# Kernel optimization log

Measured on AMD Instinct MI355X. Metric: run time of the kernel, lower is better.

Reference implementation:

```python
import jax, jax.numpy as jnp
import numpy as np

DIM = 1024
NUM_HEADS = 16
HEAD_DIM = DIM // NUM_HEADS
B, S, E = 4, 8192, 2000


def setup_inputs() -> dict:
    key = jax.random.key(0)
    ks = jax.random.split(key, 16)
    sd = 0.02
    inp = {
        "x": jax.random.normal(ks[0], (B, S, DIM), dtype=jnp.float32),
        "src_indices": jax.random.randint(ks[1], (E,), 0, S),
        "dst_indices": jax.random.randint(ks[2], (E,), 0, S),
        # linear weights stored [in, out] (applied as x @ W + b)
        "Wq": jax.random.normal(ks[3], (DIM, DIM), jnp.float32) * sd,
        "bq": jnp.zeros((DIM,), jnp.float32),
        "Wk": jax.random.normal(ks[4], (DIM, DIM), jnp.float32) * sd,
        "bk": jnp.zeros((DIM,), jnp.float32),
        "Wv": jax.random.normal(ks[5], (DIM, DIM), jnp.float32) * sd,
        "bv": jnp.zeros((DIM,), jnp.float32),
        "Wo": jax.random.normal(ks[6], (DIM, DIM), jnp.float32) * sd,
        "bo": jnp.zeros((DIM,), jnp.float32),
        "edge_weight": jax.random.normal(ks[7], (1, NUM_HEADS, 1), jnp.float32),
        "W1": jax.random.normal(ks[8], (2 * HEAD_DIM, HEAD_DIM), jnp.float32) * sd,
        "b1": jnp.zeros((HEAD_DIM,), jnp.float32),
        "W2": jax.random.normal(ks[9], (HEAD_DIM, 1), jnp.float32) * sd,
        "b2": jnp.zeros((1,), jnp.float32),
    }
    return inp


def reference(x, src_indices, dst_indices, Wq, bq, Wk, bk, Wv, bv, Wo, bo,
              edge_weight, W1, b1, W2, b2):
    Bs, Sl, D = x.shape
    H, hd = NUM_HEADS, HEAD_DIM
    scale = hd ** -0.5

    def heads(t):  # [B,S,D] -> [B,H,S,hd]
        return t.reshape(Bs, Sl, H, hd).transpose(0, 2, 1, 3)

    q = heads(x @ Wq + bq)
    k = heads(x @ Wk + bk)
    v = heads(x @ Wv + bv)

    q_src = jnp.take(q, src_indices, axis=2)   # [B,H,E,hd]
    k_dst = jnp.take(k, dst_indices, axis=2)   # [B,H,E,hd]
    v_dst = jnp.take(v, dst_indices, axis=2)   # [B,H,E,hd]

    ef = jnp.concatenate([q_src, k_dst], axis=-1)          # [B,H,E,2hd]
    h = jax.nn.gelu(ef @ W1 + b1, approximate=False)       # [B,H,E,hd]
    scores = (h @ W2 + b2) * scale                         # [B,H,E,1]
    attn = jax.nn.softmax(scores, axis=2)                  # softmax over all edges
    attn = attn * edge_weight[..., None]                   # [1,H,1,1] broadcast

    weighted = attn * v_dst                                # [B,H,E,hd]
    out = jnp.zeros((Bs, H, Sl, hd), x.dtype).at[:, :, src_indices, :].add(weighted)

    final = out.transpose(0, 2, 1, 3).reshape(Bs, Sl, D)
    return final @ Wo + bo
```

## Files before the change

### kernel.cpp

```cpp
#include <hip/hip_runtime.h>
#include <hip/hip_bf16.h>
#include <math.h>

#define DIMK 1024
#define NH 16
#define HD 64
#define BB 4
#define SS 8192
#define EPAD 136
#define NKT 32

typedef __attribute__((ext_vector_type(8))) short bf16x8;
typedef __attribute__((ext_vector_type(8))) unsigned short ushort8;
typedef __attribute__((ext_vector_type(4))) unsigned short us4;
typedef __attribute__((ext_vector_type(4))) float f32x4;

#define MFMA16(a, b, c) __builtin_amdgcn_mfma_f32_16x16x32_bf16((a), (b), (c), 0, 0, 0)

__device__ __forceinline__ unsigned short f32_to_bf16_rne(float f) {
  unsigned int u = __float_as_uint(f);
  u = (u + 0x7fffu + ((u >> 16) & 1u)) >> 16;
  return (unsigned short)u;
}
__device__ __forceinline__ float bf16_bits_to_f32(unsigned short b) {
  return __uint_as_float(((unsigned int)b) << 16);
}
__device__ __forceinline__ void gload16(const void* g, void* l) {
  __builtin_amdgcn_global_load_lds((const __attribute__((address_space(1))) void*)g,
                                   (__attribute__((address_space(3))) void*)l, 16, 0, 0);
}

__global__ __launch_bounds__(256) void fill_out_kernel(const float4* __restrict__ bo4,
                                                       float4* __restrict__ out, int total4) {
  for (int i = blockIdx.x * 256 + threadIdx.x; i < total4; i += gridDim.x * 256)
    out[i] = bo4[i & 255];
}

__global__ __launch_bounds__(256) void prep_w4(
    const float* __restrict__ Wq, const float* __restrict__ Wk,
    const float* __restrict__ Wv, const float* __restrict__ Wo,
    unsigned short* __restrict__ Bq, unsigned short* __restrict__ Bkv,
    unsigned short* __restrict__ Bo) {
  const float* W;
  unsigned short* Bpan;
  int pnoff;
  switch (blockIdx.z) {
    case 0: W = Wq; Bpan = Bq; pnoff = 0; break;
    case 1: W = Wk; Bpan = Bkv; pnoff = 0; break;
    case 2: W = Wv; Bpan = Bkv; pnoff = 8; break;
    default: W = Wo; Bpan = Bo; pnoff = 0; break;
  }
  __shared__ float st[64][65];
  const int bk = blockIdx.x * 64, bn = blockIdx.y * 64;
  const int t = threadIdx.x;
  const int lr = t >> 4, lc = (t & 15) * 4;
#pragma unroll
  for (int i = 0; i < 4; i++) {
    int k = lr + i * 16;
    float4 v = *(const float4*)(W + (size_t)(bk + k) * DIMK + bn + lc);
    st[k][lc] = v.x; st[k][lc + 1] = v.y; st[k][lc + 2] = v.z; st[k][lc + 3] = v.w;
  }
  __syncthreads();
  const int ktile = (bk + lc) >> 5, c = lc & 31;
#pragma unroll
  for (int i = 0; i < 4; i++) {
    const int nl = lr + i * 16;
    const int n = bn + nl;
    const int r = n & 127, pn = (n >> 7) + pnoff;
    const int q = (c >> 3) ^ ((r >> 1) & 3);
    const size_t byteoff = (size_t)r * 64 + q * 16 + (c & 7) * 2;
    us4 hv, lv;
#pragma unroll
    for (int j = 0; j < 4; j++) {
      float v = st[lc + j][nl];
      unsigned short hb = f32_to_bf16_rne(v);
      hv[j] = hb;
      lv[j] = f32_to_bf16_rne(v - bf16_bits_to_f32(hb));
    }
    char* base = (char*)Bpan;
    *(us4*)(base + (((size_t)pn * 64 + ktile) << 13) + byteoff) = hv;
    *(us4*)(base + (((size_t)pn * 64 + 32 + ktile) << 13) + byteoff) = lv;
  }
}

__global__ __launch_bounds__(256) void prep_w1(const float* __restrict__ W1,
                                               unsigned short* __restrict__ W1Th,
                                               unsigned short* __restrict__ W1Tl) {
  for (int idx = threadIdx.x; idx < 128 * 64; idx += 256) {
    int k = idx >> 6, n = idx & 63;
    float v = W1[idx];
    unsigned short hb = f32_to_bf16_rne(v);
    W1Th[n * 128 + k] = hb;
    W1Tl[n * 128 + k] = f32_to_bf16_rne(v - bf16_bits_to_f32(hb));
  }
}

__global__ __launch_bounds__(256) void prep_a(const float* __restrict__ X,
                                              const int* __restrict__ gidx,
                                              unsigned short* __restrict__ Apan, int M, int E) {
  const int row = blockIdx.x;
  const int r = row & 255, mt = row >> 8;
  const int c0 = threadIdx.x * 4;
  const int kt = c0 >> 5, c = c0 & 31;
  const int q = (c >> 3) ^ ((r >> 1) & 3);
  const size_t byteoff = (size_t)r * 64 + q * 16 + (c & 7) * 2;
  char* base = (char*)Apan;
  us4 hv = (us4){0, 0, 0, 0}, lv = (us4){0, 0, 0, 0};
  if (row < M) {
    const float* sr;
    if (gidx) {
      int b = row / E, e = row - b * E;
      sr = X + ((size_t)b * SS + gidx[e]) * DIMK;
    } else {
      sr = X + (size_t)row * DIMK;
    }
    float4 v = *(const float4*)(sr + c0);
    float vv[4] = {v.x, v.y, v.z, v.w};
#pragma unroll
    for (int i = 0; i < 4; i++) {
      unsigned short hb = f32_to_bf16_rne(vv[i]);
      hv[i] = hb;
      lv[i] = f32_to_bf16_rne(vv[i] - bf16_bits_to_f32(hb));
    }
  }
  *(us4*)(base + (((size_t)(mt * 64 + kt)) << 14) + byteoff) = hv;
  *(us4*)(base + (((size_t)(mt * 64 + 32 + kt)) << 14) + byteoff) = lv;
}

__global__ __launch_bounds__(1024) void first_occ(const int* __restrict__ src,
                                                  int* __restrict__ fidx,
                                                  int* __restrict__ mark, int E) {
  __shared__ int tbl[SS];
  for (int i = threadIdx.x; i < SS; i += 1024) tbl[i] = 0x7fffffff;
  __syncthreads();
  for (int e = threadIdx.x; e < E; e += 1024) atomicMin(&tbl[src[e]], e);
  __syncthreads();
  for (int e = threadIdx.x; e < E; e += 1024) mark[e] = 0;
  __syncthreads();
  for (int e = threadIdx.x; e < E; e += 1024) {
    int f = tbl[src[e]];
    fidx[e] = f;
    if (f != e) mark[f] = 1;
  }
}

template <int BN, int MODE>
__global__ __launch_bounds__(512, 2) void gemm8(
    const unsigned short* __restrict__ Apan, const unsigned short* __restrict__ Bpan,
    const float* __restrict__ bias, const float* __restrict__ bias2,
    float* __restrict__ out, int ldc, int nty,
    const int* __restrict__ fidx, const int* __restrict__ srci, int M, int E) {
  constexpr int NF = BN / 64;
  constexpr int BT = BN * 32;
  __shared__ unsigned short ldsAh[2][8192];
  __shared__ unsigned short ldsAl[2][8192];
  __shared__ unsigned short ldsBh[2][BT];
  __shared__ unsigned short ldsBl[2][BT];

  const int tid = threadIdx.x, lane = tid & 63, wv = tid >> 6;
  const int wr = wv >> 2, wc = wv & 3;

  const int w = (blockIdx.x & 7) * ((int)gridDim.x >> 3) + ((int)blockIdx.x >> 3);
  const int mt = w / nty, nt_ = w - mt * nty;
  const int m0 = mt * 256, n0 = nt_ * BN;

  const int rr = lane & 15, lq = lane >> 4;
  const int swz = (rr >> 1) & 3;
  const int aoff = (wr * 128 + rr) * 32 + ((lq ^ swz) << 3);
  const int boff = (wc * (BN / 4) + rr) * 32 + ((lq ^ swz) << 3);

  const char* Apb = (const char*)Apan + ((size_t)(mt * 64) << 14);
  const char* Bpb = (const char*)Bpan;
  const int stoff = wv * 1024 + lane * 16;

  f32x4 acc[8][NF];
#pragma unroll
  for (int i = 0; i < 8; i++)
#pragma unroll
    for (int j = 0; j < NF; j++) acc[i][j] = (f32x4){0.f, 0.f, 0.f, 0.f};

  auto stage = [&](int kt, int buf) {
    const char* sAh = Apb + ((size_t)kt << 14) + stoff;
    const char* sAl = Apb + ((size_t)(32 + kt) << 14) + stoff;
    gload16(sAh, &ldsAh[buf][wv * 512]);
    gload16(sAh + 8192, &ldsAh[buf][wv * 512 + 4096]);
    gload16(sAl, &ldsAl[buf][wv * 512]);
    gload16(sAl + 8192, &ldsAl[buf][wv * 512 + 4096]);
    if (BN == 256) {
      const char* sB0h = Bpb + (((size_t)(2 * nt_) * 64 + kt) << 13) + stoff;
      const char* sB1h = Bpb + (((size_t)(2 * nt_ + 1) * 64 + kt) << 13) + stoff;
      const char* sB0l = Bpb + (((size_t)(2 * nt_) * 64 + 32 + kt) << 13) + stoff;
      const char* sB1l = Bpb + (((size_t)(2 * nt_ + 1) * 64 + 32 + kt) << 13) + stoff;
      gload16(sB0h, &ldsBh[buf][wv * 512]);
      gload16(sB1h, &ldsBh[buf][wv * 512 + 4096]);
      gload16(sB0l, &ldsBl[buf][wv * 512]);
      gload16(sB1l, &ldsBl[buf][wv * 512 + 4096]);
    } else {
      const char* sBh = Bpb + (((size_t)nt_ * 64 + kt) << 13) + stoff;
      const char* sBl = Bpb + (((size_t)nt_ * 64 + 32 + kt) << 13) + stoff;
      gload16(sBh, &ldsBh[buf][wv * 512]);
      gload16(sBl, &ldsBl[buf][wv * 512]);
    }
  };

  stage(0, 0);
  asm volatile("s_waitcnt vmcnt(0)" ::: "memory");
  __builtin_amdgcn_sched_barrier(0);
  __builtin_amdgcn_s_barrier();

  for (int kt = 0; kt < NKT; ++kt) {
    const int buf = kt & 1;
    const unsigned short* Ah = ldsAh[buf];
    const unsigned short* Al = ldsAl[buf];
    const unsigned short* Bh = ldsBh[buf];
    const unsigned short* Bl = ldsBl[buf];

    bf16x8 fbh[NF], fah[8], fal[8], fbl[NF];
#pragma unroll
    for (int nf = 0; nf < NF; ++nf) fbh[nf] = *(const bf16x8*)(Bh + boff + nf * 512);
#pragma unroll
    for (int mf = 0; mf < 8; ++mf) fah[mf] = *(const bf16x8*)(Ah + aoff + mf * 512);
    __builtin_amdgcn_sched_barrier(0);
#pragma unroll
    for (int mf = 0; mf < 8; ++mf) fal[mf] = *(const bf16x8*)(Al + aoff + mf * 512);
    __builtin_amdgcn_sched_barrier(0);
#pragma unroll
    for (int nf = 0; nf < NF; ++nf) fbl[nf] = *(const bf16x8*)(Bl + boff + nf * 512);
    __builtin_amdgcn_sched_barrier(0);

    if (kt + 1 < NKT) stage(kt + 1, buf ^ 1);

    asm volatile("s_waitcnt lgkmcnt(%0)" ::"i"(8 + NF) : "memory");
    __builtin_amdgcn_sched_barrier(0);
    __builtin_amdgcn_s_setprio(1);
#pragma unroll
    for (int mf = 0; mf < 8; ++mf)
#pragma unroll
      for (int nf = 0; nf < NF; ++nf) acc[mf][nf] = MFMA16(fah[mf], fbh[nf], acc[mf][nf]);
    __builtin_amdgcn_s_setprio(0);

    asm volatile("s_waitcnt lgkmcnt(%0)" ::"i"(NF) : "memory");
    __builtin_amdgcn_sched_barrier(0);
    __builtin_amdgcn_s_setprio(1);
#pragma unroll
    for (int mf = 0; mf < 8; ++mf)
#pragma unroll
      for (int nf = 0; nf < NF; ++nf) acc[mf][nf] = MFMA16(fal[mf], fbh[nf], acc[mf][nf]);
    __builtin_amdgcn_s_setprio(0);

    asm volatile("s_waitcnt lgkmcnt(0)" ::: "memory");
    if (kt + 1 < NKT) {
      asm volatile("s_waitcnt vmcnt(0)" ::: "memory");
      __builtin_amdgcn_sched_barrier(0);
      __builtin_amdgcn_s_barrier();
    } else {
      __builtin_amdgcn_sched_barrier(0);
    }

    __builtin_amdgcn_s_setprio(1);
#pragma unroll
    for (int mf = 0; mf < 8; ++mf)
#pragma unroll
      for (int nf = 0; nf < NF; ++nf) acc[mf][nf] = MFMA16(fah[mf], fbl[nf], acc[mf][nf]);
    __builtin_amdgcn_s_setprio(0);
  }

  const int cq = lane >> 4, cr = lane & 15;
#pragma unroll
  for (int nf = 0; nf < NF; ++nf) {
    const int col = n0 + wc * (BN / 4) + nf * 16 + cr;
    const float bv = (MODE == 0 && bias2 != nullptr && col >= DIMK) ? bias2[col - DIMK]
                                                                    : bias[col & (DIMK - 1)];
#pragma unroll
    for (int mf = 0; mf < 8; ++mf) {
#pragma unroll
      for (int r = 0; r < 4; ++r) {
        const int mrow = m0 + wr * 128 + mf * 16 + cq * 4 + r;
        if (mrow >= M) continue;
        if (MODE == 0) {
          out[(size_t)mrow * ldc + col] = acc[mf][nf][r] + bv;
        } else {
          int b = mrow / E, e = mrow - b * E;
          if (fidx[e] == e) {
            int orow = b * SS + srci[e];
            out[(size_t)orow * ldc + col] = acc[mf][nf][r] + bv;
          }
        }
      }
    }
  }
}

__global__ __launch_bounds__(256) void edge_scores_mfma(
    const float* __restrict__ qs, const float* __restrict__ kd, int ldk,
    const unsigned short* __restrict__ W1Th, const unsigned short* __restrict__ W1Tl,
    const float* __restrict__ b1, const float* __restrict__ W2,
    const float* __restrict__ b2, float* __restrict__ scores, int E, int CH) {
  __shared__ unsigned short W1h[64][EPAD], W1l[64][EPAD];
  __shared__ unsigned short EFh[4][16][EPAD], EFl[4][16][EPAD];
  const int tid = threadIdx.x, lane = tid & 63, w = tid >> 6;
  const int bh = blockIdx.x / CH, ch = blockIdx.x - bh * CH;
  const int b = bh >> 4, h = bh & 15;

  for (int idx = tid; idx < 64 * 16; idx += 256) {
    int n = idx >> 4, g = (idx & 15) * 8;
    *(ushort8*)&W1h[n][g] = *(const ushort8*)(W1Th + n * 128 + g);
    *(ushort8*)&W1l[n][g] = *(const ushort8*)(W1Tl + n * 128 + g);
  }
  __syncthreads();

  const int etile = ch * 4 + w;
  const int e0 = etile * 16;
  if (e0 >= E) return;

  const int r = lane >> 2, c0 = (lane & 3) * 16;
  {
    const int er = (e0 + r < E) ? e0 + r : E - 1;
    const float* qrow = qs + ((size_t)(b * E + er)) * DIMK + h * HD + c0;
    const float* krow = kd + ((size_t)(b * E + er)) * (size_t)ldk + h * HD + c0;
    float qv[16], kvv[16];
#pragma unroll
    for (int i = 0; i < 4; i++) {
      *(float4*)&qv[i * 4] = *(const float4*)(qrow + i * 4);
      *(float4*)&kvv[i * 4] = *(const float4*)(krow + i * 4);
    }
    ushort8 qh[2], ql[2], kh[2], kl[2];
#pragma unroll
    for (int g = 0; g < 2; g++)
#pragma unroll
      for (int i = 0; i < 8; i++) {
        float v = qv[g * 8 + i];
        unsigned short hb = f32_to_bf16_rne(v);
        qh[g][i] = hb;
        ql[g][i] = f32_to_bf16_rne(v - bf16_bits_to_f32(hb));
        float v2 = kvv[g * 8 + i];
        unsigned short hb2 = f32_to_bf16_rne(v2);
        kh[g][i] = hb2;
        kl[g][i] = f32_to_bf16_rne(v2 - bf16_bits_to_f32(hb2));
      }
    *(ushort8*)&EFh[w][r][c0] = qh[0];
    *(ushort8*)&EFh[w][r][c0 + 8] = qh[1];
    *(ushort8*)&EFl[w][r][c0] = ql[0];
    *(ushort8*)&EFl[w][r][c0 + 8] = ql[1];
    *(ushort8*)&EFh[w][r][64 + c0] = kh[0];
    *(ushort8*)&EFh[w][r][64 + c0 + 8] = kh[1];
    *(ushort8*)&EFl[w][r][64 + c0] = kl[0];
    *(ushort8*)&EFl[w][r][64 + c0 + 8] = kl[1];
  }
  asm volatile("s_waitcnt lgkmcnt(0)" ::: "memory");
  __builtin_amdgcn_sched_barrier(0);

  f32x4 acc[4];
#pragma unroll
  for (int i = 0; i < 4; i++) acc[i] = (f32x4){0.f, 0.f, 0.f, 0.f};

  const int kk = (lane >> 4) * 8, rrl = lane & 15;
#pragma unroll
  for (int ks = 0; ks < 4; ks++) {
    bf16x8 ah = *(bf16x8*)&EFh[w][rrl][ks * 32 + kk];
    bf16x8 al = *(bf16x8*)&EFl[w][rrl][ks * 32 + kk];
#pragma unroll
    for (int nf = 0; nf < 4; nf++) {
      bf16x8 bh_ = *(bf16x8*)&W1h[nf * 16 + rrl][ks * 32 + kk];
      bf16x8 bl_ = *(bf16x8*)&W1l[nf * 16 + rrl][ks * 32 + kk];
      acc[nf] = MFMA16(ah, bh_, acc[nf]);
      acc[nf] = MFMA16(ah, bl_, acc[nf]);
      acc[nf] = MFMA16(al, bh_, acc[nf]);
    }
  }

  const int col_l = lane & 15, rq = lane >> 4;
  float w2v[4], b1v[4];
#pragma unroll
  for (int nf = 0; nf < 4; nf++) {
    w2v[nf] = W2[nf * 16 + col_l];
    b1v[nf] = b1[nf * 16 + col_l];
  }
  float p[4];
#pragma unroll
  for (int rr2 = 0; rr2 < 4; rr2++) {
    float s = 0.f;
#pragma unroll
    for (int nf = 0; nf < 4; nf++) {
      float hv = acc[nf][rr2] + b1v[nf];
      hv = 0.5f * hv * (1.f + erff(hv * 0.70710678118654752f));
      s = fmaf(hv, w2v[nf], s);
    }
    p[rr2] = s;
  }
#pragma unroll
  for (int off = 1; off < 16; off <<= 1)
#pragma unroll
    for (int rr2 = 0; rr2 < 4; rr2++) p[rr2] += __shfl_xor(p[rr2], off, 64);

  if (col_l == 0) {
    const float b2v = b2[0];
#pragma unroll
    for (int rr2 = 0; rr2 < 4; rr2++) {
      int e = e0 + rq * 4 + rr2;
      if (e < E) scores[(size_t)(b * NH + h) * E + e] = (p[rr2] + b2v) * 0.125f;
    }
  }
}

__global__ __launch_bounds__(256) void softmax_ew(float* __restrict__ scores,
                                                  const float* __restrict__ ew, int E) {
  const int row = blockIdx.x;
  const int h = row & (NH - 1);
  float* s = scores + (size_t)row * E;
  const int tid = threadIdx.x, lane = tid & 63, w = tid >> 6;
  __shared__ float red[4];

  float vals[8];
  float mx = -1e30f;
#pragma unroll
  for (int i = 0; i < 8; i++) {
    int j = tid + i * 256;
    vals[i] = (j < E) ? s[j] : -1e30f;
    mx = fmaxf(mx, vals[i]);
  }
#pragma unroll
  for (int off = 32; off; off >>= 1) mx = fmaxf(mx, __shfl_xor(mx, off, 64));
  if (lane == 0) red[w] = mx;
  __syncthreads();
  mx = fmaxf(fmaxf(red[0], red[1]), fmaxf(red[2], red[3]));
  __syncthreads();

  float sum = 0.f;
#pragma unroll
  for (int i = 0; i < 8; i++) {
    vals[i] = __expf(vals[i] - mx);
    if (tid + i * 256 < E) sum += vals[i];
  }
#pragma unroll
  for (int off = 32; off; off >>= 1) sum += __shfl_xor(sum, off, 64);
  if (lane == 0) red[w] = sum;
  __syncthreads();
  sum = red[0] + red[1] + red[2] + red[3];

  const float scaleout = ew[h] / sum;
#pragma unroll
  for (int i = 0; i < 8; i++) {
    int j = tid + i * 256;
    if (j < E) s[j] = vals[i] * scaleout;
  }
}

__global__ __launch_bounds__(256) void weight_split(
    const float* __restrict__ vd, int ldv, const float* __restrict__ attn,
    float* __restrict__ wrow, unsigned short* __restrict__ Apan, int M, int E) {
  const int row = blockIdx.x;
  const int r = row & 255, mt = row >> 8;
  const int c0 = threadIdx.x * 4;
  const int kt = c0 >> 5, c = c0 & 31;
  const int q = (c >> 3) ^ ((r >> 1) & 3);
  const size_t byteoff = (size_t)r * 64 + q * 16 + (c & 7) * 2;
  char* base = (char*)Apan;
  us4 hv = (us4){0, 0, 0, 0}, lv = (us4){0, 0, 0, 0};
  if (row < M) {
    const int b = row / E, e = row - b * E;
    const float a = attn[(size_t)(b * NH + (c0 >> 6)) * E + e];
    float4 v = *(const float4*)(vd + (size_t)row * ldv + c0);
    v.x *= a; v.y *= a; v.z *= a; v.w *= a;
    *(float4*)(wrow + (size_t)row * DIMK + c0) = v;
    float vv[4] = {v.x, v.y, v.z, v.w};
#pragma unroll
    for (int i = 0; i < 4; i++) {
      unsigned short hb = f32_to_bf16_rne(vv[i]);
      hv[i] = hb;
      lv[i] = f32_to_bf16_rne(vv[i] - bf16_bits_to_f32(hb));
    }
  }
  *(us4*)(base + (((size_t)(mt * 64 + kt)) << 14) + byteoff) = hv;
  *(us4*)(base + (((size_t)(mt * 64 + 32 + kt)) << 14) + byteoff) = lv;
}

__global__ __launch_bounds__(256) void dup_add(const int* __restrict__ f,
                                               float* __restrict__ wrow, int E) {
  const int e = blockIdx.x;
  const int fe = f[e];
  if (fe == e) return;
  const int d = threadIdx.x * 4;
#pragma unroll
  for (int b = 0; b < BB; b++) {
    const float4 v = *(const float4*)(wrow + (size_t)(b * E + e) * DIMK + d);
    float* dst = wrow + (size_t)(b * E + fe) * DIMK + d;
    atomicAdd(dst + 0, v.x);
    atomicAdd(dst + 1, v.y);
    atomicAdd(dst + 2, v.z);
    atomicAdd(dst + 3, v.w);
  }
}

__global__ __launch_bounds__(256) void dup_fix(const int* __restrict__ fidx,
                                               const int* __restrict__ mark,
                                               const float* __restrict__ wrow,
                                               unsigned short* __restrict__ Apan, int E) {
  const int e = blockIdx.x;
  if (fidx[e] != e || !mark[e]) return;
  const int c0 = threadIdx.x * 4;
  const int kt = c0 >> 5, c = c0 & 31;
  char* base = (char*)Apan;
  for (int b = 0; b < BB; b++) {
    const int row = b * E + e;
    const int r = row & 255, mt = row >> 8;
    const int q = (c >> 3) ^ ((r >> 1) & 3);
    const size_t byteoff = (size_t)r * 64 + q * 16 + (c & 7) * 2;
    float4 v = *(const float4*)(wrow + (size_t)row * DIMK + c0);
    float vv[4] = {v.x, v.y, v.z, v.w};
    us4 hv, lv;
#pragma unroll
    for (int i = 0; i < 4; i++) {
      unsigned short hb = f32_to_bf16_rne(vv[i]);
      hv[i] = hb;
      lv[i] = f32_to_bf16_rne(vv[i] - bf16_bits_to_f32(hb));
    }
    *(us4*)(base + (((size_t)(mt * 64 + kt)) << 14) + byteoff) = hv;
    *(us4*)(base + (((size_t)(mt * 64 + 32 + kt)) << 14) + byteoff) = lv;
  }
}

extern "C" void kernel_launch(void* const* d_in, const int* in_sizes, int n_in,
                              void* d_out, int out_size, void* d_ws, size_t ws_size,
                              hipStream_t stream) {
  const float* x = (const float*)d_in[0];
  const int* src = (const int*)d_in[1];
  const int* dst = (const int*)d_in[2];
  const float* Wq = (const float*)d_in[3];
  const float* bq = (const float*)d_in[4];
  const float* Wk = (const float*)d_in[5];
  const float* bk = (const float*)d_in[6];
  const float* Wv = (const float*)d_in[7];
  const float* bv = (const float*)d_in[8];
  const float* Wo = (const float*)d_in[9];
  const float* bo = (const float*)d_in[10];
  const float* ew = (const float*)d_in[11];
  const float* W1 = (const float*)d_in[12];
  const float* b1 = (const float*)d_in[13];
  const float* W2 = (const float*)d_in[14];
  const float* b2 = (const float*)d_in[15];
  float* out = (float*)d_out;

  const int E = in_sizes[1];
  const int M = BB * E;
  const int gx = (M + 255) / 256;
  const int Mpad = gx * 256;

  char* w = (char*)d_ws;
  float* qs = (float*)w; w += (size_t)M * DIMK * 4;
  float* kv = (float*)w; w += (size_t)M * 2048 * 4;
  float* sc = (float*)w; w += (size_t)BB * NH * E * 4;
  int* fidx = (int*)w; w += (((size_t)E * 4) + 255) & ~(size_t)255;
  int* mark = (int*)w; w += (((size_t)E * 4) + 255) & ~(size_t)255;
  unsigned short* W1Th = (unsigned short*)w; w += 64 * 128 * 2;
  unsigned short* W1Tl = (unsigned short*)w; w += 64 * 128 * 2;
  unsigned short* Bq = (unsigned short*)w; w += (size_t)8 * 64 * 8192;
  unsigned short* Bkv = (unsigned short*)w; w += (size_t)16 * 64 * 8192;
  unsigned short* Bo = (unsigned short*)w; w += (size_t)8 * 64 * 8192;
  unsigned short* Apan = (unsigned short*)w; w += (size_t)gx * 64 * 16384;

  float* wrow = qs;

  const int total4 = BB * SS * (DIMK / 4);
  fill_out_kernel<<<2048, 256, 0, stream>>>((const float4*)bo, (float4*)out, total4);

  prep_w4<<<dim3(16, 16, 4), 256, 0, stream>>>(Wq, Wk, Wv, Wo, Bq, Bkv, Bo);
  prep_w1<<<1, 256, 0, stream>>>(W1, W1Th, W1Tl);

  first_occ<<<1, 1024, 0, stream>>>(src, fidx, mark, E);

  prep_a<<<Mpad, 256, 0, stream>>>(x, src, Apan, M, E);
  gemm8<128, 0><<<gx * 8, 512, 0, stream>>>(Apan, Bq, bq, nullptr, qs, DIMK, 8,
                                            nullptr, nullptr, M, E);

  prep_a<<<Mpad, 256, 0, stream>>>(x, dst, Apan, M, E);
  gemm8<256, 0><<<gx * 8, 512, 0, stream>>>(Apan, Bkv, bk, bv, kv, 2048, 8,
                                            nullptr, nullptr, M, E);

  const int etiles = (E + 15) / 16;
  const int CH = (etiles + 3) / 4;
  edge_scores_mfma<<<BB * NH * CH, 256, 0, stream>>>(qs, kv, 2048, W1Th, W1Tl, b1, W2, b2,
                                                     sc, E, CH);
  softmax_ew<<<BB * NH, 256, 0, stream>>>(sc, ew, E);

  weight_split<<<Mpad, 256, 0, stream>>>(kv + 1024, 2048, sc, wrow, Apan, M, E);
  dup_add<<<E, 256, 0, stream>>>(fidx, wrow, E);
  dup_fix<<<E, 256, 0, stream>>>(fidx, mark, wrow, Apan, E);

  gemm8<128, 1><<<gx * 8, 512, 0, stream>>>(Apan, Bo, bo, nullptr, out, DIMK, 8,
                                            fidx, src, M, E);
}
```

Baseline: 344.9 us.

## Fold W1 into Q/K projection weights and simplify edge score kernel

```diff
diff --git a/kernel.cpp b/kernel.cpp
--- a/kernel.cpp
+++ b/kernel.cpp
@@ -7,7 +7,6 @@
 #define HD 64
 #define BB 4
 #define SS 8192
-#define EPAD 136
 #define NKT 32
 
 typedef __attribute__((ext_vector_type(8))) short bf16x8;
@@ -36,20 +35,12 @@
     out[i] = bo4[i & 255];
 }
 
-__global__ __launch_bounds__(256) void prep_w4(
-    const float* __restrict__ Wq, const float* __restrict__ Wk,
+__global__ __launch_bounds__(256) void prep_w2(
     const float* __restrict__ Wv, const float* __restrict__ Wo,
-    unsigned short* __restrict__ Bq, unsigned short* __restrict__ Bkv,
-    unsigned short* __restrict__ Bo) {
-  const float* W;
-  unsigned short* Bpan;
-  int pnoff;
-  switch (blockIdx.z) {
-    case 0: W = Wq; Bpan = Bq; pnoff = 0; break;
-    case 1: W = Wk; Bpan = Bkv; pnoff = 0; break;
-    case 2: W = Wv; Bpan = Bkv; pnoff = 8; break;
-    default: W = Wo; Bpan = Bo; pnoff = 0; break;
-  }
+    unsigned short* __restrict__ Bkv, unsigned short* __restrict__ Bo) {
+  const float* W = blockIdx.z ? Wo : Wv;
+  unsigned short* Bpan = blockIdx.z ? Bo : Bkv;
+  const int pnoff = blockIdx.z ? 0 : 8;
   __shared__ float st[64][65];
   const int bk = blockIdx.x * 64, bn = blockIdx.y * 64;
   const int t = threadIdx.x;
@@ -83,16 +74,70 @@
   }
 }
 
-__global__ __launch_bounds__(256) void prep_w1(const float* __restrict__ W1,
-                                               unsigned short* __restrict__ W1Th,
-                                               unsigned short* __restrict__ W1Tl) {
-  for (int idx = threadIdx.x; idx < 128 * 64; idx += 256) {
-    int k = idx >> 6, n = idx & 63;
-    float v = W1[idx];
-    unsigned short hb = f32_to_bf16_rne(v);
-    W1Th[n * 128 + k] = hb;
-    W1Tl[n * 128 + k] = f32_to_bf16_rne(v - bf16_bits_to_f32(hb));
-  }
+__global__ __launch_bounds__(256) void prep_wfold(
+    const float* __restrict__ Wq, const float* __restrict__ Wk,
+    const float* __restrict__ W1,
+    unsigned short* __restrict__ Bq, unsigned short* __restrict__ Bkv) {
+  const int which = blockIdx.z;
+  const float* W = which ? Wk : Wq;
+  unsigned short* Bpan = which ? Bkv : Bq;
+  const int d_off = which ? 64 : 0;
+  const int cc = blockIdx.x, jc = blockIdx.y;
+  __shared__ float Wb[64][65];
+  __shared__ float W1b[64][65];
+  const int t = threadIdx.x;
+  for (int idx = t; idx < 64 * 64; idx += 256) {
+    int rrow = idx >> 6, dd = idx & 63;
+    Wb[rrow][dd] = W[(size_t)(cc * 64 + rrow) * DIMK + jc * 64 + dd];
+    W1b[rrow][dd] = W1[(size_t)(d_off + rrow) * 64 + dd];
+  }
+  __syncthreads();
+  const int n = t & 63, g0 = t >> 6;
+  const int pn = jc >> 1;
+  const int r = (jc & 1) * 64 + n;
+  const int sw = (r >> 1) & 3;
+  char* base = (char*)Bpan;
+#pragma unroll
+  for (int i = 0; i < 4; ++i) {
+    const int cl0 = (g0 + 4 * i) * 4;
+    float a0 = 0.f, a1 = 0.f, a2 = 0.f, a3 = 0.f;
+    for (int d = 0; d < 64; ++d) {
+      const float w1v = W1b[d][n];
+      a0 = fmaf(Wb[cl0 + 0][d], w1v, a0);
+      a1 = fmaf(Wb[cl0 + 1][d], w1v, a1);
+      a2 = fmaf(Wb[cl0 + 2][d], w1v, a2);
+      a3 = fmaf(Wb[cl0 + 3][d], w1v, a3);
+    }
+    float av[4] = {a0, a1, a2, a3};
+    const int c = cc * 64 + cl0;
+    const int kt = c >> 5, kcol = c & 31;
+    const int q = (kcol >> 3) ^ sw;
+    const size_t byteoff = (size_t)r * 64 + q * 16 + (kcol & 7) * 2;
+    us4 hv, lv;
+#pragma unroll
+    for (int j = 0; j < 4; j++) {
+      unsigned short hb = f32_to_bf16_rne(av[j]);
+      hv[j] = hb;
+      lv[j] = f32_to_bf16_rne(av[j] - bf16_bits_to_f32(hb));
+    }
+    *(us4*)(base + (((size_t)pn * 64 + kt) << 13) + byteoff) = hv;
+    *(us4*)(base + (((size_t)pn * 64 + 32 + kt) << 13) + byteoff) = lv;
+  }
+}
+
+__global__ __launch_bounds__(256) void prep_bias(
+    const float* __restrict__ bq, const float* __restrict__ bk,
+    const float* __restrict__ b1, const float* __restrict__ W1,
+    float* __restrict__ bqf, float* __restrict__ bkf) {
+  const int j = blockIdx.x * 256 + threadIdx.x;
+  const int h = j >> 6, n = j & 63;
+  float sq = 0.f, sk = 0.f;
+  for (int d = 0; d < 64; ++d) {
+    sq = fmaf(bq[h * 64 + d], W1[d * 64 + n], sq);
+    sk = fmaf(bk[h * 64 + d], W1[(64 + d) * 64 + n], sk);
+  }
+  bqf[j] = sq;
+  bkf[j] = sk + b1[n];
 }
 
 __global__ __launch_bounds__(256) void prep_a(const float* __restrict__ X,
@@ -144,38 +189,41 @@
   }
 }
 
-template <int BN, int MODE>
-__global__ __launch_bounds__(512, 2) void gemm8(
+template <int BM, int MODE>
+__global__ __launch_bounds__(512, 2) void gemmT(
     const unsigned short* __restrict__ Apan, const unsigned short* __restrict__ Bpan,
     const float* __restrict__ bias, const float* __restrict__ bias2,
     float* __restrict__ out, int ldc, int nty,
     const int* __restrict__ fidx, const int* __restrict__ srci, int M, int E) {
-  constexpr int NF = BN / 64;
-  constexpr int BT = BN * 32;
-  __shared__ unsigned short ldsAh[2][8192];
-  __shared__ unsigned short ldsAl[2][8192];
-  __shared__ unsigned short ldsBh[2][BT];
-  __shared__ unsigned short ldsBl[2][BT];
+  constexpr int MF = BM / 32;
+  constexpr int NF = 4;
+  constexpr int AT = BM * 32;
+  __shared__ unsigned short ldsAh[2][AT];
+  __shared__ unsigned short ldsAl[2][AT];
+  __shared__ unsigned short ldsBh[2][8192];
+  __shared__ unsigned short ldsBl[2][8192];
 
   const int tid = threadIdx.x, lane = tid & 63, wv = tid >> 6;
   const int wr = wv >> 2, wc = wv & 3;
 
   const int w = (blockIdx.x & 7) * ((int)gridDim.x >> 3) + ((int)blockIdx.x >> 3);
-  const int mt = w / nty, nt_ = w - mt * nty;
-  const int m0 = mt * 256, n0 = nt_ * BN;
+  const int mi = w / nty, nt_ = w - mi * nty;
+  const int m0 = mi * BM, n0 = nt_ * 256;
 
   const int rr = lane & 15, lq = lane >> 4;
   const int swz = (rr >> 1) & 3;
-  const int aoff = (wr * 128 + rr) * 32 + ((lq ^ swz) << 3);
-  const int boff = (wc * (BN / 4) + rr) * 32 + ((lq ^ swz) << 3);
-
-  const char* Apb = (const char*)Apan + ((size_t)(mt * 64) << 14);
+  const int aoff = (wr * (BM / 2) + rr) * 32 + ((lq ^ swz) << 3);
+  const int boff = (wc * 64 + rr) * 32 + ((lq ^ swz) << 3);
+
+  const int pt = (BM == 256) ? mi : (mi >> 1);
+  const int rowbase = (BM == 256) ? 0 : (mi & 1) * 128;
+  const char* Apb = (const char*)Apan + (((size_t)pt * 64) << 14) + (size_t)rowbase * 64;
   const char* Bpb = (const char*)Bpan;
   const int stoff = wv * 1024 + lane * 16;
 
-  f32x4 acc[8][NF];
-#pragma unroll
-  for (int i = 0; i < 8; i++)
+  f32x4 acc[MF][NF];
+#pragma unroll
+  for (int i = 0; i < MF; i++)
 #pragma unroll
     for (int j = 0; j < NF; j++) acc[i][j] = (f32x4){0.f, 0.f, 0.f, 0.f};
 
@@ -183,24 +231,19 @@
     const char* sAh = Apb + ((size_t)kt << 14) + stoff;
     const char* sAl = Apb + ((size_t)(32 + kt) << 14) + stoff;
     gload16(sAh, &ldsAh[buf][wv * 512]);
-    gload16(sAh + 8192, &ldsAh[buf][wv * 512 + 4096]);
     gload16(sAl, &ldsAl[buf][wv * 512]);
-    gload16(sAl + 8192, &ldsAl[buf][wv * 512 + 4096]);
-    if (BN == 256) {
-      const char* sB0h = Bpb + (((size_t)(2 * nt_) * 64 + kt) << 13) + stoff;
-      const char* sB1h = Bpb + (((size_t)(2 * nt_ + 1) * 64 + kt) << 13) + stoff;
-      const char* sB0l = Bpb + (((size_t)(2 * nt_) * 64 + 32 + kt) << 13) + stoff;
-      const char* sB1l = Bpb + (((size_t)(2 * nt_ + 1) * 64 + 32 + kt) << 13) + stoff;
-      gload16(sB0h, &ldsBh[buf][wv * 512]);
-      gload16(sB1h, &ldsBh[buf][wv * 512 + 4096]);
-      gload16(sB0l, &ldsBl[buf][wv * 512]);
-      gload16(sB1l, &ldsBl[buf][wv * 512 + 4096]);
-    } else {
-      const char* sBh = Bpb + (((size_t)nt_ * 64 + kt) << 13) + stoff;
-      const char* sBl = Bpb + (((size_t)nt_ * 64 + 32 + kt) << 13) + stoff;
-      gload16(sBh, &ldsBh[buf][wv * 512]);
-      gload16(sBl, &ldsBl[buf][wv * 512]);
-    }
+    if (BM == 256) {
+      gload16(sAh + 8192, &ldsAh[buf][wv * 512 + 4096]);
+      gload16(sAl + 8192, &ldsAl[buf][wv * 512 + 4096]);
+    }
+    const char* sB0h = Bpb + (((size_t)(2 * nt_) * 64 + kt) << 13) + stoff;
+    const char* sB1h = Bpb + (((size_t)(2 * nt_ + 1) * 64 + kt) << 13) + stoff;
+    const char* sB0l = Bpb + (((size_t)(2 * nt_) * 64 + 32 + kt) << 13) + stoff;
+    const char* sB1l = Bpb + (((size_t)(2 * nt_ + 1) * 64 + 32 + kt) << 13) + stoff;
+    gload16(sB0h, &ldsBh[buf][wv * 512]);
+    gload16(sB1h, &ldsBh[buf][wv * 512 + 4096]);
+    gload16(sB0l, &ldsBl[buf][wv * 512]);
+    gload16(sB1l, &ldsBl[buf][wv * 512 + 4096]);
   };
 
   stage(0, 0);
@@ -215,14 +258,14 @@
     const unsigned short* Bh = ldsBh[buf];
     const unsigned short* Bl = ldsBl[buf];
 
-    bf16x8 fbh[NF], fah[8], fal[8], fbl[NF];
+    bf16x8 fbh[NF], fah[MF], fal[MF], fbl[NF];
 #pragma unroll
     for (int nf = 0; nf < NF; ++nf) fbh[nf] = *(const bf16x8*)(Bh + boff + nf * 512);
 #pragma unroll
-    for (int mf = 0; mf < 8; ++mf) fah[mf] = *(const bf16x8*)(Ah + aoff + mf * 512);
+    for (int mf = 0; mf < MF; ++mf) fah[mf] = *(const bf16x8*)(Ah + aoff + mf * 512);
     __builtin_amdgcn_sched_barrier(0);
 #pragma unroll
-    for (int mf = 0; mf < 8; ++mf) fal[mf] = *(const bf16x8*)(Al + aoff + mf * 512);
+    for (int mf = 0; mf < MF; ++mf) fal[mf] = *(const bf16x8*)(Al + aoff + mf * 512);
     __builtin_amdgcn_sched_barrier(0);
 #pragma unroll
     for (int nf = 0; nf < NF; ++nf) fbl[nf] = *(const bf16x8*)(Bl + boff + nf * 512);
@@ -230,11 +273,11 @@
 
     if (kt + 1 < NKT) stage(kt + 1, buf ^ 1);
 
-    asm volatile("s_waitcnt lgkmcnt(%0)" ::"i"(8 + NF) : "memory");
+    asm volatile("s_waitcnt lgkmcnt(%0)" ::"i"(MF + NF) : "memory");
     __builtin_amdgcn_sched_barrier(0);
     __builtin_amdgcn_s_setprio(1);
 #pragma unroll
-    for (int mf = 0; mf < 8; ++mf)
+    for (int mf = 0; mf < MF; ++mf)
 #pragma unroll
       for (int nf = 0; nf < NF; ++nf) acc[mf][nf] = MFMA16(fah[mf], fbh[nf], acc[mf][nf]);
     __builtin_amdgcn_s_setprio(0);
@@ -243,7 +286,7 @@
     __builtin_amdgcn_sched_barrier(0);
     __builtin_amdgcn_s_setprio(1);
 #pragma unroll
-    for (int mf = 0; mf < 8; ++mf)
+    for (int mf = 0; mf < MF; ++mf)
 #pragma unroll
       for (int nf = 0; nf < NF; ++nf) acc[mf][nf] = MFMA16(fal[mf], fbh[nf], acc[mf][nf]);
     __builtin_amdgcn_s_setprio(0);
@@ -259,7 +302,7 @@
 
     __builtin_amdgcn_s_setprio(1);
 #pragma unroll
-    for (int mf = 0; mf < 8; ++mf)
+    for (int mf = 0; mf < MF; ++mf)
 #pragma unroll
       for (int nf = 0; nf < NF; ++nf) acc[mf][nf] = MFMA16(fah[mf], fbl[nf], acc[mf][nf]);
     __builtin_amdgcn_s_setprio(0);
@@ -268,14 +311,14 @@
   const int cq = lane >> 4, cr = lane & 15;
 #pragma unroll
   for (int nf = 0; nf < NF; ++nf) {
-    const int col = n0 + wc * (BN / 4) + nf * 16 + cr;
+    const int col = n0 + wc * 64 + nf * 16 + cr;
     const float bv = (MODE == 0 && bias2 != nullptr && col >= DIMK) ? bias2[col - DIMK]
                                                                     : bias[col & (DIMK - 1)];
 #pragma unroll
-    for (int mf = 0; mf < 8; ++mf) {
+    for (int mf = 0; mf < MF; ++mf) {
 #pragma unroll
       for (int r = 0; r < 4; ++r) {
-        const int mrow = m0 + wr * 128 + mf * 16 + cq * 4 + r;
+        const int mrow = m0 + wr * (BM / 2) + mf * 16 + cq * 4 + r;
         if (mrow >= M) continue;
         if (MODE == 0) {
           out[(size_t)mrow * ldc + col] = acc[mf][nf][r] + bv;
@@ -291,115 +334,26 @@
   }
 }
 
-__global__ __launch_bounds__(256) void edge_scores_mfma(
-    const float* __restrict__ qs, const float* __restrict__ kd, int ldk,
-    const unsigned short* __restrict__ W1Th, const unsigned short* __restrict__ W1Tl,
-    const float* __restrict__ b1, const float* __restrict__ W2,
-    const float* __restrict__ b2, float* __restrict__ scores, int E, int CH) {
-  __shared__ unsigned short W1h[64][EPAD], W1l[64][EPAD];
-  __shared__ unsigned short EFh[4][16][EPAD], EFl[4][16][EPAD];
+__global__ __launch_bounds__(256) void edge_scores_f(
+    const float* __restrict__ hq, const float* __restrict__ hk,
+    const float* __restrict__ W2, const float* __restrict__ b2,
+    float* __restrict__ scores, int E, int CH) {
   const int tid = threadIdx.x, lane = tid & 63, w = tid >> 6;
   const int bh = blockIdx.x / CH, ch = blockIdx.x - bh * CH;
   const int b = bh >> 4, h = bh & 15;
-
-  for (int idx = tid; idx < 64 * 16; idx += 256) {
-    int n = idx >> 4, g = (idx & 15) * 8;
-    *(ushort8*)&W1h[n][g] = *(const ushort8*)(W1Th + n * 128 + g);
-    *(ushort8*)&W1l[n][g] = *(const ushort8*)(W1Tl + n * 128 + g);
-  }
-  __syncthreads();
-
-  const int etile = ch * 4 + w;
-  const int e0 = etile * 16;
-  if (e0 >= E) return;
-
-  const int r = lane >> 2, c0 = (lane & 3) * 16;
-  {
-    const int er = (e0 + r < E) ? e0 + r : E - 1;
-    const float* qrow = qs + ((size_t)(b * E + er)) * DIMK + h * HD + c0;
-    const float* krow = kd + ((size_t)(b * E + er)) * (size_t)ldk + h * HD + c0;
-    float qv[16], kvv[16];
-#pragma unroll
-    for (int i = 0; i < 4; i++) {
-      *(float4*)&qv[i * 4] = *(const float4*)(qrow + i * 4);
-      *(float4*)&kvv[i * 4] = *(const float4*)(krow + i * 4);
-    }
-    ushort8 qh[2], ql[2], kh[2], kl[2];
-#pragma unroll
-    for (int g = 0; g < 2; g++)
-#pragma unroll
-      for (int i = 0; i < 8; i++) {
-        float v = qv[g * 8 + i];
-        unsigned short hb = f32_to_bf16_rne(v);
-        qh[g][i] = hb;
-        ql[g][i] = f32_to_bf16_rne(v - bf16_bits_to_f32(hb));
-        float v2 = kvv[g * 8 + i];
-        unsigned short hb2 = f32_to_bf16_rne(v2);
-        kh[g][i] = hb2;
-        kl[g][i] = f32_to_bf16_rne(v2 - bf16_bits_to_f32(hb2));
-      }
-    *(ushort8*)&EFh[w][r][c0] = qh[0];
-    *(ushort8*)&EFh[w][r][c0 + 8] = qh[1];
-    *(ushort8*)&EFl[w][r][c0] = ql[0];
-    *(ushort8*)&EFl[w][r][c0 + 8] = ql[1];
-    *(ushort8*)&EFh[w][r][64 + c0] = kh[0];
-    *(ushort8*)&EFh[w][r][64 + c0 + 8] = kh[1];
-    *(ushort8*)&EFl[w][r][64 + c0] = kl[0];
-    *(ushort8*)&EFl[w][r][64 + c0 + 8] = kl[1];
-  }
-  asm volatile("s_waitcnt lgkmcnt(0)" ::: "memory");
-  __builtin_amdgcn_sched_barrier(0);
-
-  f32x4 acc[4];
-#pragma unroll
-  for (int i = 0; i < 4; i++) acc[i] = (f32x4){0.f, 0.f, 0.f, 0.f};
-
-  const int kk = (lane >> 4) * 8, rrl = lane & 15;
-#pragma unroll
-  for (int ks = 0; ks < 4; ks++) {
-    bf16x8 ah = *(bf16x8*)&EFh[w][rrl][ks * 32 + kk];
-    bf16x8 al = *(bf16x8*)&EFl[w][rrl][ks * 32 + kk];
-#pragma unroll
-    for (int nf = 0; nf < 4; nf++) {
-      bf16x8 bh_ = *(bf16x8*)&W1h[nf * 16 + rrl][ks * 32 + kk];
-      bf16x8 bl_ = *(bf16x8*)&W1l[nf * 16 + rrl][ks * 32 + kk];
-      acc[nf] = MFMA16(ah, bh_, acc[nf]);
-      acc[nf] = MFMA16(ah, bl_, acc[nf]);
-      acc[nf] = MFMA16(al, bh_, acc[nf]);
-    }
-  }
-
-  const int col_l = lane & 15, rq = lane >> 4;
-  float w2v[4], b1v[4];
-#pragma unroll
-  for (int nf = 0; nf < 4; nf++) {
-    w2v[nf] = W2[nf * 16 + col_l];
-    b1v[nf] = b1[nf * 16 + col_l];
-  }
-  float p[4];
-#pragma unroll
-  for (int rr2 = 0; rr2 < 4; rr2++) {
-    float s = 0.f;
-#pragma unroll
-    for (int nf = 0; nf < 4; nf++) {
-      float hv = acc[nf][rr2] + b1v[nf];
-      hv = 0.5f * hv * (1.f + erff(hv * 0.70710678118654752f));
-      s = fmaf(hv, w2v[nf], s);
-    }
-    p[rr2] = s;
-  }
-#pragma unroll
-  for (int off = 1; off < 16; off <<= 1)
-#pragma unroll
-    for (int rr2 = 0; rr2 < 4; rr2++) p[rr2] += __shfl_xor(p[rr2], off, 64);
-
-  if (col_l == 0) {
-    const float b2v = b2[0];
-#pragma unroll
-    for (int rr2 = 0; rr2 < 4; rr2++) {
-      int e = e0 + rq * 4 + rr2;
-      if (e < E) scores[(size_t)(b * NH + h) * E + e] = (p[rr2] + b2v) * 0.125f;
-    }
+  const float w2 = W2[lane];
+  const float b2v = b2[0];
+#pragma unroll
+  for (int i = 0; i < 8; ++i) {
+    const int e = ch * 32 + w * 8 + i;
+    if (e >= E) break;
+    const size_t row = (size_t)(b * E + e);
+    float hv = hq[row * 1024 + h * 64 + lane] + hk[row * 2048 + h * 64 + lane];
+    hv = 0.5f * hv * (1.f + erff(hv * 0.70710678118654752f));
+    float p = hv * w2;
+#pragma unroll
+    for (int off = 32; off; off >>= 1) p += __shfl_xor(p, off, 64);
+    if (lane == 0) scores[(size_t)(b * NH + h) * E + e] = (p + b2v) * 0.125f;
   }
 }
 
@@ -545,6 +499,7 @@
   const int M = BB * E;
   const int gx = (M + 255) / 256;
   const int Mpad = gx * 256;
+  const int mi128 = gx * 2;
 
   char* w = (char*)d_ws;
   float* qs = (float*)w; w += (size_t)M * DIMK * 4;
@@ -552,8 +507,8 @@
   float* sc = (float*)w; w += (size_t)BB * NH * E * 4;
   int* fidx = (int*)w; w += (((size_t)E * 4) + 255) & ~(size_t)255;
   int* mark = (int*)w; w += (((size_t)E * 4) + 255) & ~(size_t)255;
-  unsigned short* W1Th = (unsigned short*)w; w += 64 * 128 * 2;
-  unsigned short* W1Tl = (unsigned short*)w; w += 64 * 128 * 2;
+  float* bqf = (float*)w; w += 1024 * 4;
+  float* bkf = (float*)w; w += 1024 * 4;
   unsigned short* Bq = (unsigned short*)w; w += (size_t)8 * 64 * 8192;
   unsigned short* Bkv = (unsigned short*)w; w += (size_t)16 * 64 * 8192;
   unsigned short* Bo = (unsigned short*)w; w += (size_t)8 * 64 * 8192;
@@ -564,29 +519,28 @@
   const int total4 = BB * SS * (DIMK / 4);
   fill_out_kernel<<<2048, 256, 0, stream>>>((const float4*)bo, (float4*)out, total4);
 
-  prep_w4<<<dim3(16, 16, 4), 256, 0, stream>>>(Wq, Wk, Wv, Wo, Bq, Bkv, Bo);
-  prep_w1<<<1, 256, 0, stream>>>(W1, W1Th, W1Tl);
+  prep_w2<<<dim3(16, 16, 2), 256, 0, stream>>>(Wv, Wo, Bkv, Bo);
+  prep_wfold<<<dim3(16, 16, 2), 256, 0, stream>>>(Wq, Wk, W1, Bq, Bkv);
+  prep_bias<<<4, 256, 0, stream>>>(bq, bk, b1, W1, bqf, bkf);
 
   first_occ<<<1, 1024, 0, stream>>>(src, fidx, mark, E);
 
   prep_a<<<Mpad, 256, 0, stream>>>(x, src, Apan, M, E);
-  gemm8<128, 0><<<gx * 8, 512, 0, stream>>>(Apan, Bq, bq, nullptr, qs, DIMK, 8,
+  gemmT<128, 0><<<mi128 * 4, 512, 0, stream>>>(Apan, Bq, bqf, nullptr, qs, DIMK, 4,
+                                               nullptr, nullptr, M, E);
+
+  prep_a<<<Mpad, 256, 0, stream>>>(x, dst, Apan, M, E);
+  gemmT<256, 0><<<gx * 8, 512, 0, stream>>>(Apan, Bkv, bkf, bv, kv, 2048, 8,
                                             nullptr, nullptr, M, E);
 
-  prep_a<<<Mpad, 256, 0, stream>>>(x, dst, Apan, M, E);
-  gemm8<256, 0><<<gx * 8, 512, 0, stream>>>(Apan, Bkv, bk, bv, kv, 2048, 8,
-                                            nullptr, nullptr, M, E);
-
-  const int etiles = (E + 15) / 16;
-  const int CH = (etiles + 3) / 4;
-  edge_scores_mfma<<<BB * NH * CH, 256, 0, stream>>>(qs, kv, 2048, W1Th, W1Tl, b1, W2, b2,
-                                                     sc, E, CH);
+  const int CH = (E + 31) / 32;
+  edge_scores_f<<<BB * NH * CH, 256, 0, stream>>>(qs, kv, W2, b2, sc, E, CH);
   softmax_ew<<<BB * NH, 256, 0, stream>>>(sc, ew, E);
 
   weight_split<<<Mpad, 256, 0, stream>>>(kv + 1024, 2048, sc, wrow, Apan, M, E);
   dup_add<<<E, 256, 0, stream>>>(fidx, wrow, E);
   dup_fix<<<E, 256, 0, stream>>>(fidx, mark, wrow, Apan, E);
 
-  gemm8<128, 1><<<gx * 8, 512, 0, stream>>>(Apan, Bo, bo, nullptr, out, DIMK, 8,
-                                            fidx, src, M, E);
-}
+  gemmT<128, 1><<<mi128 * 4, 512, 0, stream>>>(Apan, Bo, bo, nullptr, out, DIMK, 4,
+                                               fidx, src, M, E);
+}
```

Measured after the change: 334.2 us, median of 2. 1.03x faster.
